# Performance work log

Hardware: AMD Instinct MI355X
Metric: run time of the kernel (lower is better)

## Reference

```python
import jax, jax.numpy as jnp
import numpy as np

N_NODES = 50000
N_EDGES = 600000
D = 128


def setup_inputs() -> dict:
    key = jax.random.key(0)
    k1, k2, k3, k4, k5 = jax.random.split(key, 5)
    node_feats = jax.random.normal(k1, (N_NODES, D), dtype=jnp.float32)
    edge_feats = jax.random.normal(k2, (N_EDGES, D), dtype=jnp.float32)
    mlp_w = jax.random.normal(k3, (D, D), dtype=jnp.float32) * (1.0 / np.sqrt(D))
    mlp_b = jnp.zeros((D,), dtype=jnp.float32)
    scale = jnp.ones((D,), dtype=jnp.float32) * 0.1  # LayerScale init_eps for depth<=18
    src = jax.random.randint(k4, (N_EDGES,), 0, N_NODES, dtype=jnp.int64)
    dst = jax.random.randint(k5, (N_EDGES,), 0, N_NODES, dtype=jnp.int64)
    return {"node_feats": node_feats, "edge_feats": edge_feats, "mlp_w": mlp_w,
            "mlp_b": mlp_b, "scale": scale, "src": src, "dst": dst}


def reference(node_feats, edge_feats, mlp_w, mlp_b, scale, src, dst):
    n = node_feats.shape[0]
    # u_add_e: gather source node feats, add edge feats -> per-edge message m [E, D]
    m = node_feats[src] + edge_feats
    # edge_softmax: per-destination-node, per-channel softmax over incoming edges
    mx = jax.ops.segment_max(m, dst, num_segments=n)        # [N, D] (-inf for empty)
    ex = jnp.exp(m - mx[dst])                               # [E, D]
    denom = jax.ops.segment_sum(ex, dst, num_segments=n)    # [N, D]
    a = ex / denom[dst]                                     # [E, D]
    # weighted scatter-sum aggregation: sum_e m * a -> [N, D]
    agg = jax.ops.segment_sum(m * a, dst, num_segments=n)
    # MLP -> activation -> (dropout=identity) -> LayerScale -> residual
    h = jax.nn.relu(agg @ mlp_w.T + mlp_b)
    return h * scale + node_feats
```

## Files before the change

kernel.cpp:

```cpp
#include <hip/hip_runtime.h>

#define NNODES 50000
#define NEDGES 600000
#define DIM 128
#define BSTRIDE 64

typedef float f32x4 __attribute__((ext_vector_type(4)));

__device__ __forceinline__ float bf2f(unsigned short v) {
    return __uint_as_float(((unsigned int)v) << 16);
}
__device__ __forceinline__ unsigned short f2bf(float f) {
    unsigned int b = __float_as_uint(f);
    return (unsigned short)((b + 0x7fff + ((b >> 16) & 1)) >> 16);
}


__global__ __launch_bounds__(256) void k_setup(const float* __restrict__ nf,
                                               ushort* __restrict__ nf16,
                                               int* __restrict__ cursor) {
    int i = blockIdx.x * 256 + threadIdx.x;
    if (i < NNODES * DIM / 4) {
        f32x4 v = *reinterpret_cast<const f32x4*>(&nf[(size_t)i * 4]);
        ushort4 o;
        o.x = f2bf(v.x); o.y = f2bf(v.y); o.z = f2bf(v.z); o.w = f2bf(v.w);
        *reinterpret_cast<ushort4*>(&nf16[(size_t)i * 4]) = o;
    }
    if (i < NNODES) cursor[i] = 0;
}

__global__ __launch_bounds__(256) void k_scatter(const int* __restrict__ src,
                                                 const int* __restrict__ dst,
                                                 int* __restrict__ cursor,
                                                 int2* __restrict__ pairs) {
    int e = blockIdx.x * 256 + threadIdx.x;
    if (e < NEDGES) {
        int d = dst[e];
        int pos = atomicAdd(&cursor[d], 1);
        if (pos < BSTRIDE)
            pairs[((size_t)d << 6) + pos] = make_int2(e, src[e]);
    }
}

__global__ __launch_bounds__(256) void k_agg(
    const ushort* __restrict__ nf16, const float* __restrict__ ef,
    const int* __restrict__ cursor, const int2* __restrict__ pairs,
    ushort* __restrict__ agg16)
{
    const int wid = threadIdx.x >> 6, lane = threadIdx.x & 63;
    const int n = blockIdx.x * 4 + wid;
    if (n >= NNODES) return;
    const int dg = min(cursor[n], BSTRIDE);
    const int beg = n << 6;
    const int half = lane >> 5;
    const int c = (lane & 31) << 2;

    float d0 = 0.f, d1 = 0.f, d2 = 0.f, d3 = 0.f;
    float w0 = 0.f, w1 = 0.f, w2 = 0.f, w3 = 0.f;

    int2 mp = make_int2(0, 0);
    if (lane < dg) mp = pairs[beg + lane];
    const int meid = mp.x, msrc = mp.y;

    int b = 0;
    for (; b + 8 <= dg; b += 8) {
        const int i0 = b + (half << 2);
        int e0 = __shfl(meid, i0),     s0 = __shfl(msrc, i0);
        int e1 = __shfl(meid, i0 + 1), s1 = __shfl(msrc, i0 + 1);
        int e2 = __shfl(meid, i0 + 2), s2 = __shfl(msrc, i0 + 2);
        int e3 = __shfl(meid, i0 + 3), s3 = __shfl(msrc, i0 + 3);
        const ushort4 a0 = *reinterpret_cast<const ushort4*>(&nf16[(size_t)s0 * DIM + c]);
        const f32x4 b0 = __builtin_nontemporal_load(
            reinterpret_cast<const f32x4*>(&ef[(size_t)e0 * DIM + c]));
        const ushort4 a1 = *reinterpret_cast<const ushort4*>(&nf16[(size_t)s1 * DIM + c]);
        const f32x4 b1 = __builtin_nontemporal_load(
            reinterpret_cast<const f32x4*>(&ef[(size_t)e1 * DIM + c]));
        const ushort4 a2 = *reinterpret_cast<const ushort4*>(&nf16[(size_t)s2 * DIM + c]);
        const f32x4 b2 = __builtin_nontemporal_load(
            reinterpret_cast<const f32x4*>(&ef[(size_t)e2 * DIM + c]));
        const ushort4 a3 = *reinterpret_cast<const ushort4*>(&nf16[(size_t)s3 * DIM + c]);
        const f32x4 b3 = __builtin_nontemporal_load(
            reinterpret_cast<const f32x4*>(&ef[(size_t)e3 * DIM + c]));
        #pragma unroll
        for (int q = 0; q < 4; ++q) {
            ushort4 a = q == 0 ? a0 : (q == 1 ? a1 : (q == 2 ? a2 : a3));
            f32x4 bb = q == 0 ? b0 : (q == 1 ? b1 : (q == 2 ? b2 : b3));
            float m0 = bf2f(a.x) + bb.x, m1 = bf2f(a.y) + bb.y,
                  m2 = bf2f(a.z) + bb.z, m3 = bf2f(a.w) + bb.w;
            float p0 = __expf(m0), p1 = __expf(m1),
                  p2 = __expf(m2), p3 = __expf(m3);
            d0 += p0; d1 += p1; d2 += p2; d3 += p3;
            w0 = fmaf(m0, p0, w0); w1 = fmaf(m1, p1, w1);
            w2 = fmaf(m2, p2, w2); w3 = fmaf(m3, p3, w3);
        }
    }
    for (; b < dg; b += 2) {
        const int idx = b + half;
        if (idx < dg) {
            int e0 = __shfl(meid, idx), s0 = __shfl(msrc, idx);
            const ushort4 a = *reinterpret_cast<const ushort4*>(&nf16[(size_t)s0 * DIM + c]);
            const f32x4 bb = __builtin_nontemporal_load(
                reinterpret_cast<const f32x4*>(&ef[(size_t)e0 * DIM + c]));
            float m0 = bf2f(a.x) + bb.x, m1 = bf2f(a.y) + bb.y,
                  m2 = bf2f(a.z) + bb.z, m3 = bf2f(a.w) + bb.w;
            float p0 = __expf(m0), p1 = __expf(m1),
                  p2 = __expf(m2), p3 = __expf(m3);
            d0 += p0; d1 += p1; d2 += p2; d3 += p3;
            w0 = fmaf(m0, p0, w0); w1 = fmaf(m1, p1, w1);
            w2 = fmaf(m2, p2, w2); w3 = fmaf(m3, p3, w3);
        }
    }

    d0 += __shfl_xor(d0, 32); d1 += __shfl_xor(d1, 32);
    d2 += __shfl_xor(d2, 32); d3 += __shfl_xor(d3, 32);
    w0 += __shfl_xor(w0, 32); w1 += __shfl_xor(w1, 32);
    w2 += __shfl_xor(w2, 32); w3 += __shfl_xor(w3, 32);
    if (half == 0) {
        ushort4 o;
        o.x = f2bf(d0 > 0.f ? w0 / d0 : 0.f);
        o.y = f2bf(d1 > 0.f ? w1 / d1 : 0.f);
        o.z = f2bf(d2 > 0.f ? w2 / d2 : 0.f);
        o.w = f2bf(d3 > 0.f ? w3 / d3 : 0.f);
        *reinterpret_cast<ushort4*>(&agg16[(size_t)n * DIM + c]) = o;
    }
}

#define GNODES 16
#define GROUPS 4
#define NODES_PER_BLOCK (GNODES * GROUPS)

__global__ __launch_bounds__(256) void k_final(
    const ushort* __restrict__ agg16,
    const float* __restrict__ W, const float* __restrict__ bias,
    const float* __restrict__ scale, const float* __restrict__ nf,
    float* __restrict__ out)
{
    __shared__ float Wt[DIM][132];
    __shared__ float aggS[GNODES][132];
    const int t = threadIdx.x;

    for (int i = t; i < DIM * DIM; i += 256) {
        Wt[i & 127][i >> 7] = W[i];
    }

    const int j4 = (t & 31) << 2;
    const float4 b4 = *reinterpret_cast<const float4*>(&bias[j4]);
    const float4 s4 = *reinterpret_cast<const float4*>(&scale[j4]);
    const int nl2 = (t >> 5) << 1;

    int base = blockIdx.x * NODES_PER_BLOCK;
    for (int g = 0; g < GROUPS; ++g, base += GNODES) {
        __syncthreads();

        {
            int f  = t << 3;
            int nl = f >> 7;
            int k  = f & 127;
            int n  = base + nl;
            if (n < NNODES) {
                uint4 v = *reinterpret_cast<const uint4*>(&agg16[(size_t)n * DIM + k]);
                aggS[nl][k + 0] = __uint_as_float(v.x << 16);
                aggS[nl][k + 1] = __uint_as_float(v.x & 0xffff0000u);
                aggS[nl][k + 2] = __uint_as_float(v.y << 16);
                aggS[nl][k + 3] = __uint_as_float(v.y & 0xffff0000u);
                aggS[nl][k + 4] = __uint_as_float(v.z << 16);
                aggS[nl][k + 5] = __uint_as_float(v.z & 0xffff0000u);
                aggS[nl][k + 6] = __uint_as_float(v.w << 16);
                aggS[nl][k + 7] = __uint_as_float(v.w & 0xffff0000u);
            } else {
                #pragma unroll
                for (int q = 0; q < 8; ++q) aggS[nl][k + q] = 0.f;
            }
        }
        __syncthreads();

        float4 accA = b4, accB = b4;
        const float* arA = aggS[nl2];
        const float* arB = aggS[nl2 + 1];
        #pragma unroll 8
        for (int k = 0; k < DIM; ++k) {
            const float4 w = *reinterpret_cast<const float4*>(&Wt[k][j4]);
            float aA = arA[k], aB = arB[k];
            accA.x = fmaf(aA, w.x, accA.x);
            accA.y = fmaf(aA, w.y, accA.y);
            accA.z = fmaf(aA, w.z, accA.z);
            accA.w = fmaf(aA, w.w, accA.w);
            accB.x = fmaf(aB, w.x, accB.x);
            accB.y = fmaf(aB, w.y, accB.y);
            accB.z = fmaf(aB, w.z, accB.z);
            accB.w = fmaf(aB, w.w, accB.w);
        }

        const int nA = base + nl2;
        const int nB = nA + 1;
        if (nA < NNODES) {
            float4 r = *reinterpret_cast<const float4*>(&nf[(size_t)nA * DIM + j4]);
            f32x4 o;
            o.x = fmaxf(accA.x, 0.f) * s4.x + r.x;
            o.y = fmaxf(accA.y, 0.f) * s4.y + r.y;
            o.z = fmaxf(accA.z, 0.f) * s4.z + r.z;
            o.w = fmaxf(accA.w, 0.f) * s4.w + r.w;
            __builtin_nontemporal_store(o,
                reinterpret_cast<f32x4*>(&out[(size_t)nA * DIM + j4]));
        }
        if (nB < NNODES) {
            float4 r = *reinterpret_cast<const float4*>(&nf[(size_t)nB * DIM + j4]);
            f32x4 o;
            o.x = fmaxf(accB.x, 0.f) * s4.x + r.x;
            o.y = fmaxf(accB.y, 0.f) * s4.y + r.y;
            o.z = fmaxf(accB.z, 0.f) * s4.z + r.z;
            o.w = fmaxf(accB.w, 0.f) * s4.w + r.w;
            __builtin_nontemporal_store(o,
                reinterpret_cast<f32x4*>(&out[(size_t)nB * DIM + j4]));
        }
    }
}

extern "C" void kernel_launch(void* const* d_in, const int* in_sizes, int n_in,
                              void* d_out, int out_size, void* d_ws, size_t ws_size,
                              hipStream_t stream) {
    const float* nf  = (const float*)d_in[0];
    const float* ef  = (const float*)d_in[1];
    const float* W   = (const float*)d_in[2];
    const float* b   = (const float*)d_in[3];
    const float* sc  = (const float*)d_in[4];
    const int*   src = (const int*)d_in[5];
    const int*   dst = (const int*)d_in[6];
    float* out = (float*)d_out;

    int2*   pairs  = (int2*)d_ws;
    int*    cursor = (int*)(pairs + (size_t)NNODES * 64);
    ushort* agg16  = (ushort*)(cursor + NNODES);
    ushort* nf16   = agg16 + (size_t)NNODES * DIM;

    k_setup  <<<(NNODES * DIM / 4 + 255) / 256, 256, 0, stream>>>(nf, nf16, cursor);
    k_scatter<<<(NEDGES + 255) / 256, 256, 0, stream>>>(src, dst, cursor, pairs);
    k_agg    <<<(NNODES + 3) / 4, 256, 0, stream>>>(nf16, ef, cursor, pairs, agg16);
    k_final  <<<(NNODES + NODES_PER_BLOCK - 1) / NODES_PER_BLOCK, 256, 0, stream>>>(
        agg16, W, b, sc, nf, out);
}
```

Measured before the change: 160.9 us.

## Fuse setup and scatter kernels, switch bf16 to fp16, use one-wave agg blocks

Merges the node-feature conversion and the edge scatter into one prep kernel, and zeroes the cursor with hipMemsetAsync instead of inside a kernel. Replaces the bf16 encoding of node features and the aggregate with fp16 using native conversions, and converts eight values per thread. The aggregation kernel now launches one 64-thread block per node instead of four nodes per 256-thread block. The aim is to save a launch and conversion instructions. The risks are fp16 range overflow and more scheduling overhead from small blocks.

```diff
diff --git a/kernel.cpp b/kernel.cpp
--- a/kernel.cpp
+++ b/kernel.cpp
@@ -5,51 +5,42 @@
 #define DIM 128
 #define BSTRIDE 64
 
-typedef float f32x4 __attribute__((ext_vector_type(4)));
-
-__device__ __forceinline__ float bf2f(unsigned short v) {
-    return __uint_as_float(((unsigned int)v) << 16);
-}
-__device__ __forceinline__ unsigned short f2bf(float f) {
-    unsigned int b = __float_as_uint(f);
-    return (unsigned short)((b + 0x7fff + ((b >> 16) & 1)) >> 16);
-}
-
-
-__global__ __launch_bounds__(256) void k_setup(const float* __restrict__ nf,
-                                               ushort* __restrict__ nf16,
-                                               int* __restrict__ cursor) {
+typedef float    f32x4 __attribute__((ext_vector_type(4)));
+typedef _Float16 f16x4 __attribute__((ext_vector_type(4)));
+typedef _Float16 f16x8 __attribute__((ext_vector_type(8)));
+
+
+__global__ __launch_bounds__(256) void k_prep(
+    const float* __restrict__ nf, _Float16* __restrict__ nfh,
+    const int* __restrict__ src, const int* __restrict__ dst,
+    int* __restrict__ cursor, int2* __restrict__ pairs)
+{
     int i = blockIdx.x * 256 + threadIdx.x;
-    if (i < NNODES * DIM / 4) {
-        f32x4 v = *reinterpret_cast<const f32x4*>(&nf[(size_t)i * 4]);
-        ushort4 o;
-        o.x = f2bf(v.x); o.y = f2bf(v.y); o.z = f2bf(v.z); o.w = f2bf(v.w);
-        *reinterpret_cast<ushort4*>(&nf16[(size_t)i * 4]) = o;
-    }
-    if (i < NNODES) cursor[i] = 0;
-}
-
-__global__ __launch_bounds__(256) void k_scatter(const int* __restrict__ src,
-                                                 const int* __restrict__ dst,
-                                                 int* __restrict__ cursor,
-                                                 int2* __restrict__ pairs) {
-    int e = blockIdx.x * 256 + threadIdx.x;
-    if (e < NEDGES) {
-        int d = dst[e];
+    if (i < NEDGES) {
+        int d = dst[i];
         int pos = atomicAdd(&cursor[d], 1);
         if (pos < BSTRIDE)
-            pairs[((size_t)d << 6) + pos] = make_int2(e, src[e]);
-    }
-}
-
-__global__ __launch_bounds__(256) void k_agg(
-    const ushort* __restrict__ nf16, const float* __restrict__ ef,
+            pairs[((size_t)d << 6) + pos] = make_int2(i, src[i]);
+    }
+    if (i < NNODES * DIM / 8) {
+        f32x4 v0 = *reinterpret_cast<const f32x4*>(&nf[(size_t)i * 8]);
+        f32x4 v1 = *reinterpret_cast<const f32x4*>(&nf[(size_t)i * 8 + 4]);
+        f16x8 o;
+        o[0] = (_Float16)v0.x; o[1] = (_Float16)v0.y;
+        o[2] = (_Float16)v0.z; o[3] = (_Float16)v0.w;
+        o[4] = (_Float16)v1.x; o[5] = (_Float16)v1.y;
+        o[6] = (_Float16)v1.z; o[7] = (_Float16)v1.w;
+        *reinterpret_cast<f16x8*>(&nfh[(size_t)i * 8]) = o;
+    }
+}
+
+__global__ __launch_bounds__(64) void k_agg(
+    const _Float16* __restrict__ nfh, const float* __restrict__ ef,
     const int* __restrict__ cursor, const int2* __restrict__ pairs,
-    ushort* __restrict__ agg16)
+    _Float16* __restrict__ aggh)
 {
-    const int wid = threadIdx.x >> 6, lane = threadIdx.x & 63;
-    const int n = blockIdx.x * 4 + wid;
-    if (n >= NNODES) return;
+    const int lane = threadIdx.x;
+    const int n = blockIdx.x;
     const int dg = min(cursor[n], BSTRIDE);
     const int beg = n << 6;
     const int half = lane >> 5;
@@ -69,24 +60,24 @@
         int e1 = __shfl(meid, i0 + 1), s1 = __shfl(msrc, i0 + 1);
         int e2 = __shfl(meid, i0 + 2), s2 = __shfl(msrc, i0 + 2);
         int e3 = __shfl(meid, i0 + 3), s3 = __shfl(msrc, i0 + 3);
-        const ushort4 a0 = *reinterpret_cast<const ushort4*>(&nf16[(size_t)s0 * DIM + c]);
+        const f16x4 a0 = *reinterpret_cast<const f16x4*>(&nfh[(size_t)s0 * DIM + c]);
         const f32x4 b0 = __builtin_nontemporal_load(
             reinterpret_cast<const f32x4*>(&ef[(size_t)e0 * DIM + c]));
-        const ushort4 a1 = *reinterpret_cast<const ushort4*>(&nf16[(size_t)s1 * DIM + c]);
+        const f16x4 a1 = *reinterpret_cast<const f16x4*>(&nfh[(size_t)s1 * DIM + c]);
         const f32x4 b1 = __builtin_nontemporal_load(
             reinterpret_cast<const f32x4*>(&ef[(size_t)e1 * DIM + c]));
-        const ushort4 a2 = *reinterpret_cast<const ushort4*>(&nf16[(size_t)s2 * DIM + c]);
+        const f16x4 a2 = *reinterpret_cast<const f16x4*>(&nfh[(size_t)s2 * DIM + c]);
         const f32x4 b2 = __builtin_nontemporal_load(
             reinterpret_cast<const f32x4*>(&ef[(size_t)e2 * DIM + c]));
-        const ushort4 a3 = *reinterpret_cast<const ushort4*>(&nf16[(size_t)s3 * DIM + c]);
+        const f16x4 a3 = *reinterpret_cast<const f16x4*>(&nfh[(size_t)s3 * DIM + c]);
         const f32x4 b3 = __builtin_nontemporal_load(
             reinterpret_cast<const f32x4*>(&ef[(size_t)e3 * DIM + c]));
         #pragma unroll
         for (int q = 0; q < 4; ++q) {
-            ushort4 a = q == 0 ? a0 : (q == 1 ? a1 : (q == 2 ? a2 : a3));
+            f16x4 a = q == 0 ? a0 : (q == 1 ? a1 : (q == 2 ? a2 : a3));
             f32x4 bb = q == 0 ? b0 : (q == 1 ? b1 : (q == 2 ? b2 : b3));
-            float m0 = bf2f(a.x) + bb.x, m1 = bf2f(a.y) + bb.y,
-                  m2 = bf2f(a.z) + bb.z, m3 = bf2f(a.w) + bb.w;
+            float m0 = (float)a.x + bb.x, m1 = (float)a.y + bb.y,
+                  m2 = (float)a.z + bb.z, m3 = (float)a.w + bb.w;
             float p0 = __expf(m0), p1 = __expf(m1),
                   p2 = __expf(m2), p3 = __expf(m3);
             d0 += p0; d1 += p1; d2 += p2; d3 += p3;
@@ -98,11 +89,11 @@
         const int idx = b + half;
         if (idx < dg) {
             int e0 = __shfl(meid, idx), s0 = __shfl(msrc, idx);
-            const ushort4 a = *reinterpret_cast<const ushort4*>(&nf16[(size_t)s0 * DIM + c]);
+            const f16x4 a = *reinterpret_cast<const f16x4*>(&nfh[(size_t)s0 * DIM + c]);
             const f32x4 bb = __builtin_nontemporal_load(
                 reinterpret_cast<const f32x4*>(&ef[(size_t)e0 * DIM + c]));
-            float m0 = bf2f(a.x) + bb.x, m1 = bf2f(a.y) + bb.y,
-                  m2 = bf2f(a.z) + bb.z, m3 = bf2f(a.w) + bb.w;
+            float m0 = (float)a.x + bb.x, m1 = (float)a.y + bb.y,
+                  m2 = (float)a.z + bb.z, m3 = (float)a.w + bb.w;
             float p0 = __expf(m0), p1 = __expf(m1),
                   p2 = __expf(m2), p3 = __expf(m3);
             d0 += p0; d1 += p1; d2 += p2; d3 += p3;
@@ -116,12 +107,12 @@
     w0 += __shfl_xor(w0, 32); w1 += __shfl_xor(w1, 32);
     w2 += __shfl_xor(w2, 32); w3 += __shfl_xor(w3, 32);
     if (half == 0) {
-        ushort4 o;
-        o.x = f2bf(d0 > 0.f ? w0 / d0 : 0.f);
-        o.y = f2bf(d1 > 0.f ? w1 / d1 : 0.f);
-        o.z = f2bf(d2 > 0.f ? w2 / d2 : 0.f);
-        o.w = f2bf(d3 > 0.f ? w3 / d3 : 0.f);
-        *reinterpret_cast<ushort4*>(&agg16[(size_t)n * DIM + c]) = o;
+        f16x4 o;
+        o.x = (_Float16)(d0 > 0.f ? w0 / d0 : 0.f);
+        o.y = (_Float16)(d1 > 0.f ? w1 / d1 : 0.f);
+        o.z = (_Float16)(d2 > 0.f ? w2 / d2 : 0.f);
+        o.w = (_Float16)(d3 > 0.f ? w3 / d3 : 0.f);
+        *reinterpret_cast<f16x4*>(&aggh[(size_t)n * DIM + c]) = o;
     }
 }
 
@@ -130,7 +121,7 @@
 #define NODES_PER_BLOCK (GNODES * GROUPS)
 
 __global__ __launch_bounds__(256) void k_final(
-    const ushort* __restrict__ agg16,
+    const _Float16* __restrict__ aggh,
     const float* __restrict__ W, const float* __restrict__ bias,
     const float* __restrict__ scale, const float* __restrict__ nf,
     float* __restrict__ out)
@@ -158,18 +149,12 @@
             int k  = f & 127;
             int n  = base + nl;
             if (n < NNODES) {
-                uint4 v = *reinterpret_cast<const uint4*>(&agg16[(size_t)n * DIM + k]);
-                aggS[nl][k + 0] = __uint_as_float(v.x << 16);
-                aggS[nl][k + 1] = __uint_as_float(v.x & 0xffff0000u);
-                aggS[nl][k + 2] = __uint_as_float(v.y << 16);
-                aggS[nl][k + 3] = __uint_as_float(v.y & 0xffff0000u);
-                aggS[nl][k + 4] = __uint_as_float(v.z << 16);
-                aggS[nl][k + 5] = __uint_as_float(v.z & 0xffff0000u);
-                aggS[nl][k + 6] = __uint_as_float(v.w << 16);
-                aggS[nl][k + 7] = __uint_as_float(v.w & 0xffff0000u);
+                f16x8 v = *reinterpret_cast<const f16x8*>(&aggh[(size_t)n * DIM + k]);
+                #pragma unroll
+                for (int j = 0; j < 8; ++j) aggS[nl][k + j] = (float)v[j];
             } else {
                 #pragma unroll
-                for (int q = 0; q < 8; ++q) aggS[nl][k + q] = 0.f;
+                for (int j = 0; j < 8; ++j) aggS[nl][k + j] = 0.f;
             }
         }
         __syncthreads();
@@ -228,14 +213,15 @@
     const int*   dst = (const int*)d_in[6];
     float* out = (float*)d_out;
 
-    int2*   pairs  = (int2*)d_ws;
-    int*    cursor = (int*)(pairs + (size_t)NNODES * 64);
-    ushort* agg16  = (ushort*)(cursor + NNODES);
-    ushort* nf16   = agg16 + (size_t)NNODES * DIM;
-
-    k_setup  <<<(NNODES * DIM / 4 + 255) / 256, 256, 0, stream>>>(nf, nf16, cursor);
-    k_scatter<<<(NEDGES + 255) / 256, 256, 0, stream>>>(src, dst, cursor, pairs);
-    k_agg    <<<(NNODES + 3) / 4, 256, 0, stream>>>(nf16, ef, cursor, pairs, agg16);
-    k_final  <<<(NNODES + NODES_PER_BLOCK - 1) / NODES_PER_BLOCK, 256, 0, stream>>>(
-        agg16, W, b, sc, nf, out);
-}
+    int2*     pairs  = (int2*)d_ws;
+    int*      cursor = (int*)(pairs + (size_t)NNODES * 64);
+    _Float16* aggh   = (_Float16*)(cursor + NNODES);
+    _Float16* nfh    = aggh + (size_t)NNODES * DIM;
+
+    hipMemsetAsync(cursor, 0, NNODES * sizeof(int), stream);
+    k_prep <<<(NNODES * DIM / 8 + 255) / 256, 256, 0, stream>>>(
+        nf, nfh, src, dst, cursor, pairs);
+    k_agg  <<<NNODES, 64, 0, stream>>>(nfh, ef, cursor, pairs, aggh);
+    k_final<<<(NNODES + NODES_PER_BLOCK - 1) / NODES_PER_BLOCK, 256, 0, stream>>>(
+        aggh, W, b, sc, nf, out);
+}
```

After: 163.1 us. No clear change (+1.4%).
